# Performance work log

Hardware: AMD Instinct MI355X
Metric: run time of the kernel (lower is better)

The kernel has to match this reference:

```python
import jax, jax.numpy as jnp
import numpy as np

B, L, E, H = 2, 2048, 1024, 16
D = E // H  # head dim = 64


def setup_inputs() -> dict:
    key = jax.random.key(0)
    ks = jax.random.split(key, 10)
    s = 0.02
    return {
        "xt": jax.random.normal(ks[0], (B, L, E), jnp.float32),
        "xs": jax.random.normal(ks[1], (B, L, E), jnp.float32),
        "Wt": jax.random.normal(ks[2], (E, 3 * E), jnp.float32) * s,  # t_attn weight (x @ Wt)
        "bt": jnp.zeros((3 * E,), jnp.float32),
        "Ws": jax.random.normal(ks[3], (E, 2 * E), jnp.float32) * s,  # s_attn weight
        "bs": jnp.zeros((2 * E,), jnp.float32),
        "Wc": jax.random.normal(ks[4], (E, E), jnp.float32) * s,      # c_proj weight
        "bc": jnp.zeros((E,), jnp.float32),
        "lam_ts": jnp.ones((1,), jnp.float32),
        "lam_st": jnp.ones((1,), jnp.float32),
        "lam_ss": jnp.ones((1,), jnp.float32),
    }


def _heads(x):
    # (B, L, E) -> (B, H, L, D)
    return x.reshape(B, L, H, D).transpose(0, 2, 1, 3)


def reference(xt, xs, Wt, bt, Ws, bs, Wc, bc, lam_ts, lam_st, lam_ss):
    qt, kt, vt = jnp.split(xt @ Wt + bt, 3, axis=2)
    qs, ks = jnp.split(xs @ Ws + bs, 2, axis=2)
    qt, kt, vt, qs, ks = map(_heads, (qt, kt, vt, qs, ks))

    # 4-way disentangled scores; fuse the 4 matmuls into 2 by combining keys:
    # qt@kt^T + lam_ts*qt@ks^T = qt @ (kt + lam_ts*ks)^T
    # lam_st*qs@kt^T + lam_ss*qs@ks^T = qs @ (lam_st*kt + lam_ss*ks)^T
    k1 = kt + lam_ts[0] * ks
    k2 = lam_st[0] * kt + lam_ss[0] * ks
    att = (jnp.einsum('bhqd,bhkd->bhqk', qt, k1)
           + jnp.einsum('bhqd,bhkd->bhqk', qs, k2)) * (1.0 / np.sqrt(D))
    att = jax.nn.softmax(att, axis=-1)
    y = jnp.einsum('bhqk,bhkd->bhqd', att, vt)  # (B, H, L, D)
    y = y.transpose(0, 2, 1, 3).reshape(B, L, E)
    return y @ Wc + bc
```

## Files before the change

kernel.cpp:

```cpp
#include <hip/hip_runtime.h>
#include <math.h>

#define LQ 2048
#define EQ 1024
#define M_ROWS 4096
#define BH 32

typedef _Float16 f16x8 __attribute__((ext_vector_type(8)));
typedef _Float16 f16x4 __attribute__((ext_vector_type(4)));
typedef _Float16 f16x2 __attribute__((ext_vector_type(2)));
typedef float f32x4 __attribute__((ext_vector_type(4)));
typedef float f32x16 __attribute__((ext_vector_type(16)));

#define QSCALE 0.1803368801111204f

__device__ __forceinline__ void async_ld16(const _Float16* g, _Float16* l) {
  __builtin_amdgcn_global_load_lds(
      (const __attribute__((address_space(1))) unsigned int*)g,
      (__attribute__((address_space(3))) unsigned int*)l, 16, 0, 0);
}

__global__ __launch_bounds__(256) void prep(
    const float* __restrict__ xt, const float* __restrict__ xs,
    const float* __restrict__ Wt, const float* __restrict__ Ws,
    const float* __restrict__ Wc,
    _Float16* __restrict__ xt16, _Float16* __restrict__ xs16,
    _Float16* __restrict__ WtT, _Float16* __restrict__ WsT,
    _Float16* __restrict__ WcT) {
  int gb = blockIdx.x;
  if (gb < 4096) {
    int i = gb * 256 + threadIdx.x;
    const float* s; _Float16* d; size_t off;
    if (i < 524288) { s = xt; d = xt16; off = (size_t)i * 8; }
    else            { s = xs; d = xs16; off = (size_t)(i - 524288) * 8; }
    float4 a = *(const float4*)&s[off];
    float4 b = *(const float4*)&s[off + 4];
    f16x8 h;
    h[0] = (_Float16)a.x; h[1] = (_Float16)a.y; h[2] = (_Float16)a.z; h[3] = (_Float16)a.w;
    h[4] = (_Float16)b.x; h[5] = (_Float16)b.y; h[6] = (_Float16)b.z; h[7] = (_Float16)b.w;
    *(f16x8*)&d[off] = h;
  } else {
    __shared__ float T[32][65];
    int tb = gb - 4096;
    int c0 = (tb % 96) * 64;
    int k0 = (tb / 96) * 32;
    const float* W; _Float16* D; int Nw, cl;
    if (c0 < 3072)      { W = Wt; D = WtT; Nw = 3072; cl = c0; }
    else if (c0 < 5120) { W = Ws; D = WsT; Nw = 2048; cl = c0 - 3072; }
    else                { W = Wc; D = WcT; Nw = 1024; cl = c0 - 5120; }
    const int tid = threadIdx.x;
#pragma unroll
    for (int p = 0; p < 4; ++p) {
      int idx = tid + p * 256;
      int row = idx >> 5;
      int c2 = (idx & 31) * 2;
      float2 v = *(const float2*)&W[(size_t)(k0 + row) * Nw + cl + c2];
      T[row][c2] = v.x;
      T[row][c2 + 1] = v.y;
    }
    __syncthreads();
#pragma unroll
    for (int p = 0; p < 4; ++p) {
      int idx = tid + p * 256;
      int col = idx >> 4;
      int k2 = (idx & 15) * 2;
      f16x2 h2;
      h2[0] = (_Float16)T[k2][col];
      h2[1] = (_Float16)T[k2 + 1][col];
      *(f16x2*)&D[(size_t)(cl + col) * 1024 + k0 + k2] = h2;
    }
  }
}

__global__ __launch_bounds__(256, 3) void proj_gemm(
    const _Float16* __restrict__ xt16, const _Float16* __restrict__ xs16,
    const _Float16* __restrict__ WtT, const _Float16* __restrict__ WsT,
    const float* __restrict__ bt, const float* __restrict__ bs,
    _Float16* __restrict__ q16, _Float16* __restrict__ k16,
    _Float16* __restrict__ v16) {
  __shared__ _Float16 Al[128 * 64];
  __shared__ _Float16 Bl[128 * 64];

  const int tid = threadIdx.x;
  const int w = tid >> 6;
  const int lane = tid & 63;
  const int quad = lane >> 4;
  const int l15 = lane & 15;
  const int wm = w >> 1, wn = w & 1;
  const int by = blockIdx.y;
  const int n0 = blockIdx.x * 128;

  const _Float16* Ab;
  const _Float16* Bb;
  const float* bias;
  int m0, bsel = 0, branch;
  if (by < 32) {
    branch = 0; Ab = xt16; Bb = WtT; bias = bt; m0 = by * 128;
  } else if (by < 48) {
    branch = 1;
    int by2 = by - 32;
    bsel = by2 >> 3;
    m0 = (by2 & 7) * 128;
    Ab = WtT + (size_t)2048 * 1024;
    Bb = xt16 + (size_t)bsel * 2048 * 1024;
    bias = bt;
  } else {
    branch = 2; Ab = xs16; Bb = WsT; bias = bs; m0 = (by - 48) * 128;
  }

  const int srow = lane >> 3;
  const int sch = lane & 7;

  f32x4 acc[4][4];
#pragma unroll
  for (int mb = 0; mb < 4; ++mb)
#pragma unroll
    for (int nb = 0; nb < 4; ++nb) acc[mb][nb] = (f32x4){0.f, 0.f, 0.f, 0.f};

  for (int kt = 0; kt < 1024; kt += 64) {
    __syncthreads();
#pragma unroll
    for (int a = 0; a < 4; ++a) {
      int row = w * 32 + a * 8 + srow;
      int sc = sch ^ (row & 7);
      async_ld16(&Ab[(size_t)(m0 + row) * 1024 + kt + sc * 8], &Al[(w * 32 + a * 8) * 64]);
      async_ld16(&Bb[(size_t)(n0 + row) * 1024 + kt + sc * 8], &Bl[(w * 32 + a * 8) * 64]);
    }
    __syncthreads();

#pragma unroll
    for (int g = 0; g < 2; ++g) {
      f16x8 af[4], bf[4];
#pragma unroll
      for (int mb = 0; mb < 4; ++mb) {
        int row = wm * 64 + mb * 16 + l15;
        int pc = ((g * 4 + quad) ^ (row & 7)) * 8;
        af[mb] = *(const f16x8*)&Al[row * 64 + pc];
      }
#pragma unroll
      for (int nb = 0; nb < 4; ++nb) {
        int row = wn * 64 + nb * 16 + l15;
        int pc = ((g * 4 + quad) ^ (row & 7)) * 8;
        bf[nb] = *(const f16x8*)&Bl[row * 64 + pc];
      }
#pragma unroll
      for (int mb = 0; mb < 4; ++mb)
#pragma unroll
        for (int nb = 0; nb < 4; ++nb)
          acc[mb][nb] = __builtin_amdgcn_mfma_f32_16x16x32_f16(af[mb], bf[nb], acc[mb][nb], 0, 0, 0);
    }
  }

#pragma unroll
  for (int mb = 0; mb < 4; ++mb)
#pragma unroll
    for (int nb = 0; nb < 4; ++nb)
#pragma unroll
      for (int r = 0; r < 4; ++r) {
        int row = m0 + wm * 64 + mb * 16 + quad * 4 + r;
        int col = n0 + wn * 64 + nb * 16 + l15;
        if (branch == 1) {
          float val = acc[mb][nb][r] + bias[2048 + row];
          v16[(size_t)(bsel * 1024 + row) * 2048 + col] = (_Float16)val;
        } else {
          float val = acc[mb][nb][r] + bias[col];
          int bb = row >> 11, ll = row & 2047;
          int which = col >> 10, e = col & 1023;
          int hh = e >> 6, dd = e & 63;
          size_t rowhd = (size_t)(bb * 16 + hh) * 2048 + ll;
          int off = (branch == 0) ? 0 : 64;
          if (which == 0) q16[rowhd * 128 + off + dd] = (_Float16)val;
          else            k16[rowhd * 128 + off + dd] = (_Float16)val;
        }
      }
}

__global__ __launch_bounds__(256, 3) void cproj_gemm(
    const _Float16* __restrict__ A, const _Float16* __restrict__ Bm,
    const float* __restrict__ bias, float* __restrict__ outf) {
  __shared__ _Float16 Al0[128 * 32];
  __shared__ _Float16 Bl0[64 * 32];
  __shared__ _Float16 Al1[128 * 32];
  __shared__ _Float16 Bl1[64 * 32];

  const int tid = threadIdx.x;
  const int w = tid >> 6;
  const int lane = tid & 63;
  const int quad = lane >> 4;
  const int l15 = lane & 15;
  const int wm = w >> 1, wn = w & 1;
  const int m0 = blockIdx.y * 128;
  const int n0 = blockIdx.x * 64;

  const int srow = lane >> 2;
  const int schunk = ((lane & 3) ^ ((lane >> 3) & 3)) * 8;

  f32x4 acc[4][2];
#pragma unroll
  for (int mb = 0; mb < 4; ++mb)
#pragma unroll
    for (int nb = 0; nb < 2; ++nb) acc[mb][nb] = (f32x4){0.f, 0.f, 0.f, 0.f};

  const int key = (l15 >> 1) & 3;

  auto dma = [&](int kt, _Float16* Al, _Float16* Bl) {
#pragma unroll
    for (int i = 0; i < 2; ++i) {
      int rt = w * 32 + i * 16;
      async_ld16(&A[(size_t)(m0 + rt + srow) * 1024 + kt + schunk], &Al[rt * 32]);
    }
    int rtb = w * 16;
    async_ld16(&Bm[(size_t)(n0 + rtb + srow) * 1024 + kt + schunk], &Bl[rtb * 32]);
  };

  auto comp = [&](const _Float16* Al, const _Float16* Bl) {
    f16x8 af[4], bf[2];
    const int pc = (quad ^ key) * 8;
#pragma unroll
    for (int mb = 0; mb < 4; ++mb)
      af[mb] = *(const f16x8*)&Al[(wm * 64 + mb * 16 + l15) * 32 + pc];
#pragma unroll
    for (int nb = 0; nb < 2; ++nb)
      bf[nb] = *(const f16x8*)&Bl[(wn * 32 + nb * 16 + l15) * 32 + pc];
#pragma unroll
    for (int mb = 0; mb < 4; ++mb)
#pragma unroll
      for (int nb = 0; nb < 2; ++nb)
        acc[mb][nb] = __builtin_amdgcn_mfma_f32_16x16x32_f16(af[mb], bf[nb], acc[mb][nb], 0, 0, 0);
  };

  dma(0, Al0, Bl0);
  for (int kt = 0; kt < 1024; kt += 64) {
    __syncthreads();
    dma(kt + 32, Al1, Bl1);
    comp(Al0, Bl0);
    __syncthreads();
    if (kt + 64 < 1024) dma(kt + 64, Al0, Bl0);
    comp(Al1, Bl1);
  }

#pragma unroll
  for (int mb = 0; mb < 4; ++mb)
#pragma unroll
    for (int nb = 0; nb < 2; ++nb)
#pragma unroll
      for (int r = 0; r < 4; ++r) {
        int row = m0 + wm * 64 + mb * 16 + quad * 4 + r;
        int col = n0 + wn * 32 + nb * 16 + l15;
        outf[(size_t)row * 1024 + col] = acc[mb][nb][r] + bias[col];
      }
}

__global__ __launch_bounds__(256, 2) void flash_attn_mfma(
    const _Float16* __restrict__ qcat, const _Float16* __restrict__ kcat,
    const _Float16* __restrict__ vT, _Float16* __restrict__ y,
    const float* __restrict__ lam_ts, const float* __restrict__ lam_st,
    const float* __restrict__ lam_ss) {
  const int bh = blockIdx.y;
  const int qt0 = blockIdx.x * 128;
  const int b = bh >> 4, h = bh & 15;
  const _Float16* Qg = qcat + (size_t)bh * LQ * 128;
  const _Float16* Kg = kcat + (size_t)bh * LQ * 128;
  const _Float16* Vg = vT + (size_t)bh * 64 * LQ;

  __shared__ _Float16 Ksh0[64 * 128];
  __shared__ _Float16 Ksh1[64 * 128];
  __shared__ _Float16 Vsh0[64 * 64];
  __shared__ _Float16 Vsh1[64 * 64];

  const int tid = threadIdx.x;
  const int w = tid >> 6;
  const int lane = tid & 63;
  const int half = lane >> 5;
  const int l31 = lane & 31;

  const float lts = lam_ts[0], lst = lam_st[0], lss = lam_ss[0];

  f16x8 qf[8];
#pragma unroll
  for (int db = 0; db < 4; ++db) {
    const _Float16* qp = &Qg[(size_t)(qt0 + w * 32 + l31) * 128 + db * 16 + half * 8];
    f16x8 a = *(const f16x8*)qp;
    f16x8 bq = *(const f16x8*)(qp + 64);
#pragma unroll
    for (int e = 0; e < 8; ++e) {
      float fa = (float)a[e], fb = (float)bq[e];
      qf[db][e]     = (_Float16)(QSCALE * (fa + lst * fb));
      qf[db + 4][e] = (_Float16)(QSCALE * (lts * fa + lss * fb));
    }
  }

  float m_i = -INFINITY;
  float l_i = 0.f;
  f32x16 O[2];
#pragma unroll
  for (int nt = 0; nt < 2; ++nt)
#pragma unroll
    for (int r = 0; r < 16; ++r) O[nt][r] = 0.f;

  auto dma = [&](int t, _Float16* Kd, _Float16* Vd) {
#pragma unroll
    for (int a = 0; a < 4; ++a) {
      int row = w * 16 + a * 4 + (lane >> 4);
      int sc = (lane & 15) ^ (row & 7);
      async_ld16(&Kg[(size_t)(t + row) * 128 + sc * 8], &Kd[(w * 16 + a * 4) * 128]);
    }
#pragma unroll
    for (int a = 0; a < 2; ++a) {
      int row = w * 16 + a * 8 + (lane >> 3);
      int sc = (lane & 7) ^ (row & 7);
      async_ld16(&Vg[(size_t)row * LQ + t + sc * 8], &Vd[(w * 16 + a * 8) * 64]);
    }
  };

  auto compute = [&](const _Float16* Ks, const _Float16* Vs) {
    f32x16 S[2];
#pragma unroll
    for (int kb = 0; kb < 2; ++kb)
#pragma unroll
      for (int r = 0; r < 16; ++r) S[kb][r] = 0.f;
#pragma unroll
    for (int db = 0; db < 8; ++db) {
      const int pc = ((db * 2 + half) ^ (lane & 7)) * 8;
      f16x8 af[2];
#pragma unroll
      for (int kb = 0; kb < 2; ++kb)
        af[kb] = *(const f16x8*)&Ks[(kb * 32 + l31) * 128 + pc];
#pragma unroll
      for (int kb = 0; kb < 2; ++kb)
        S[kb] = __builtin_amdgcn_mfma_f32_32x32x16_f16(af[kb], qf[db], S[kb], 0, 0, 0);
    }

    float mx = -INFINITY;
#pragma unroll
    for (int kb = 0; kb < 2; ++kb)
#pragma unroll
      for (int r = 0; r < 16; ++r) mx = fmaxf(mx, S[kb][r]);
    mx = fmaxf(mx, __shfl_xor(mx, 32));
    float m_new = fmaxf(m_i, mx);
    float alpha = __builtin_amdgcn_exp2f(m_i - m_new);
    float s = 0.f;
#pragma unroll
    for (int kb = 0; kb < 2; ++kb)
#pragma unroll
      for (int r = 0; r < 16; ++r) {
        float p = __builtin_amdgcn_exp2f(S[kb][r] - m_new);
        S[kb][r] = p;
        s += p;
      }
    s += __shfl_xor(s, 32);
    l_i = l_i * alpha + s;
    m_i = m_new;

#pragma unroll
    for (int nt = 0; nt < 2; ++nt)
#pragma unroll
      for (int r = 0; r < 16; ++r) O[nt][r] *= alpha;

    unsigned pu[2][8];
#pragma unroll
    for (int kb = 0; kb < 2; ++kb)
#pragma unroll
      for (int i = 0; i < 8; ++i) {
        f16x2 t2;
        t2[0] = (_Float16)S[kb][2 * i];
        t2[1] = (_Float16)S[kb][2 * i + 1];
        pu[kb][i] = __builtin_bit_cast(unsigned, t2);
      }

#pragma unroll
    for (int kb = 0; kb < 2; ++kb)
#pragma unroll
      for (int c = 0; c < 2; ++c) {
        unsigned ulo0 = pu[kb][4 * c + 0], ulo1 = pu[kb][4 * c + 1];
        unsigned uhi0 = pu[kb][4 * c + 2], uhi1 = pu[kb][4 * c + 3];
        unsigned rlo0 = (unsigned)__shfl_xor((int)ulo0, 32);
        unsigned rlo1 = (unsigned)__shfl_xor((int)ulo1, 32);
        unsigned rhi0 = (unsigned)__shfl_xor((int)uhi0, 32);
        unsigned rhi1 = (unsigned)__shfl_xor((int)uhi1, 32);
        union { unsigned u[4]; f16x8 v; } pb;
        pb.u[0] = half ? rhi0 : ulo0;
        pb.u[1] = half ? rhi1 : ulo1;
        pb.u[2] = half ? uhi0 : rlo0;
        pb.u[3] = half ? uhi1 : rlo1;
        int kb2 = kb * 2 + c;
        f16x8 av[2];
#pragma unroll
        for (int nt = 0; nt < 2; ++nt) {
          int dim = nt * 32 + l31;
          int pc = ((kb2 * 2 + half) ^ (dim & 7)) * 8;
          av[nt] = *(const f16x8*)&Vs[dim * 64 + pc];
        }
#pragma unroll
        for (int nt = 0; nt < 2; ++nt)
          O[nt] = __builtin_amdgcn_mfma_f32_32x32x16_f16(av[nt], pb.v, O[nt], 0, 0, 0);
      }
  };

  dma(0, Ksh0, Vsh0);
  for (int t = 0; t < LQ; t += 128) {
    __syncthreads();
    dma(t + 64, Ksh1, Vsh1);
    compute(Ksh0, Vsh0);
    __syncthreads();
    if (t + 128 < LQ) dma(t + 128, Ksh0, Vsh0);
    compute(Ksh1, Vsh1);
  }

  float inv = 1.f / l_i;
  int qrow = qt0 + w * 32 + l31;
#pragma unroll
  for (int nt = 0; nt < 2; ++nt)
#pragma unroll
    for (int rg = 0; rg < 4; ++rg) {
      f16x4 o4;
#pragma unroll
      for (int i = 0; i < 4; ++i) o4[i] = (_Float16)(O[nt][rg * 4 + i] * inv);
      int dim = nt * 32 + rg * 8 + half * 4;
      *(f16x4*)&y[((size_t)b * LQ + qrow) * EQ + h * 64 + dim] = o4;
    }
}

extern "C" void kernel_launch(void* const* d_in, const int* in_sizes, int n_in,
                              void* d_out, int out_size, void* d_ws, size_t ws_size,
                              hipStream_t stream) {
  const float* xt = (const float*)d_in[0];
  const float* xs = (const float*)d_in[1];
  const float* Wt = (const float*)d_in[2];
  const float* bt = (const float*)d_in[3];
  const float* Ws = (const float*)d_in[4];
  const float* bs = (const float*)d_in[5];
  const float* Wc = (const float*)d_in[6];
  const float* bc = (const float*)d_in[7];
  const float* lam_ts = (const float*)d_in[8];
  const float* lam_st = (const float*)d_in[9];
  const float* lam_ss = (const float*)d_in[10];
  float* out = (float*)d_out;

  _Float16* w16 = (_Float16*)d_ws;
  _Float16* xt16 = w16;
  _Float16* xs16 = xt16 + 4194304;
  _Float16* WtT  = xs16 + 4194304;
  _Float16* WsT  = WtT + 3145728;
  _Float16* WcT  = WsT + 2097152;
  _Float16* qcat = WcT + 1048576;
  _Float16* kcat = qcat + 8388608;
  _Float16* vbufT = kcat + 8388608;
  _Float16* ybuf = vbufT + 4194304;

  prep<<<7168, 256, 0, stream>>>(xt, xs, Wt, Ws, Wc, xt16, xs16, WtT, WsT, WcT);
  proj_gemm<<<dim3(16, 80), 256, 0, stream>>>(
      xt16, xs16, WtT, WsT, bt, bs, qcat, kcat, vbufT);
  flash_attn_mfma<<<dim3(16, 32), 256, 0, stream>>>(
      qcat, kcat, vbufT, ybuf, lam_ts, lam_st, lam_ss);
  cproj_gemm<<<dim3(16, 32), 256, 0, stream>>>(ybuf, WcT, bc, out);
}
```

Baseline: 280.9 us.

## Process 128-key blocks per softmax step with deferred rescale and permlane swaps

The attention loop now does QK^T for two 64-key tiles before running one softmax/PV pass over 128 keys. This halves the number of max/rescale passes, and it adds two more V buffers so V tiles stay resident until the PV step. Rescaling of O and l is skipped unless some row max grows by more than a threshold (lazy rescale), and MFMA sections are raised in priority with s_setprio. The cross-half P shuffle now uses v_permlane32_swap instead of four shfl_xor plus selects. The cost is more registers (S[4]) and more LDS, which could lower occupancy.

```diff
diff --git a/kernel.cpp b/kernel.cpp
--- a/kernel.cpp
+++ b/kernel.cpp
@@ -13,6 +13,7 @@
 typedef float f32x16 __attribute__((ext_vector_type(16)));
 
 #define QSCALE 0.1803368801111204f
+#define DEFER_THR 8.0f
 
 __device__ __forceinline__ void async_ld16(const _Float16* g, _Float16* l) {
   __builtin_amdgcn_global_load_lds(
@@ -267,6 +268,8 @@
   __shared__ _Float16 Ksh1[64 * 128];
   __shared__ _Float16 Vsh0[64 * 64];
   __shared__ _Float16 Vsh1[64 * 64];
+  __shared__ _Float16 Vsh2[64 * 64];
+  __shared__ _Float16 Vsh3[64 * 64];
 
   const int tid = threadIdx.x;
   const int w = tid >> 6;
@@ -298,13 +301,15 @@
 #pragma unroll
     for (int r = 0; r < 16; ++r) O[nt][r] = 0.f;
 
-  auto dma = [&](int t, _Float16* Kd, _Float16* Vd) {
+  auto dma_k = [&](int t, _Float16* Kd) {
 #pragma unroll
     for (int a = 0; a < 4; ++a) {
       int row = w * 16 + a * 4 + (lane >> 4);
       int sc = (lane & 15) ^ (row & 7);
       async_ld16(&Kg[(size_t)(t + row) * 128 + sc * 8], &Kd[(w * 16 + a * 4) * 128]);
     }
+  };
+  auto dma_v = [&](int t, _Float16* Vd) {
 #pragma unroll
     for (int a = 0; a < 2; ++a) {
       int row = w * 16 + a * 8 + (lane >> 3);
@@ -313,98 +318,112 @@
     }
   };
 
-  auto compute = [&](const _Float16* Ks, const _Float16* Vs) {
-    f32x16 S[2];
-#pragma unroll
-    for (int kb = 0; kb < 2; ++kb)
-#pragma unroll
-      for (int r = 0; r < 16; ++r) S[kb][r] = 0.f;
+  auto qk = [&](const _Float16* Ks, f32x16* Sp) {
+    __builtin_amdgcn_s_setprio(1);
 #pragma unroll
     for (int db = 0; db < 8; ++db) {
       const int pc = ((db * 2 + half) ^ (lane & 7)) * 8;
-      f16x8 af[2];
-#pragma unroll
-      for (int kb = 0; kb < 2; ++kb)
-        af[kb] = *(const f16x8*)&Ks[(kb * 32 + l31) * 128 + pc];
-#pragma unroll
-      for (int kb = 0; kb < 2; ++kb)
-        S[kb] = __builtin_amdgcn_mfma_f32_32x32x16_f16(af[kb], qf[db], S[kb], 0, 0, 0);
-    }
-
+      f16x8 af0 = *(const f16x8*)&Ks[(l31) * 128 + pc];
+      f16x8 af1 = *(const f16x8*)&Ks[(32 + l31) * 128 + pc];
+      Sp[0] = __builtin_amdgcn_mfma_f32_32x32x16_f16(af0, qf[db], Sp[0], 0, 0, 0);
+      Sp[1] = __builtin_amdgcn_mfma_f32_32x32x16_f16(af1, qf[db], Sp[1], 0, 0, 0);
+    }
+    __builtin_amdgcn_s_setprio(0);
+  };
+
+  auto softpv = [&](f32x16* S, const _Float16* Vs0, const _Float16* Vs1) {
     float mx = -INFINITY;
 #pragma unroll
-    for (int kb = 0; kb < 2; ++kb)
+    for (int kb = 0; kb < 4; ++kb)
 #pragma unroll
       for (int r = 0; r < 16; ++r) mx = fmaxf(mx, S[kb][r]);
     mx = fmaxf(mx, __shfl_xor(mx, 32));
-    float m_new = fmaxf(m_i, mx);
-    float alpha = __builtin_amdgcn_exp2f(m_i - m_new);
+
+    if (__any(mx > m_i + DEFER_THR)) {
+      float m_new = fmaxf(m_i, mx);
+      float alpha = __builtin_amdgcn_exp2f(m_i - m_new);
+      l_i *= alpha;
+#pragma unroll
+      for (int nt = 0; nt < 2; ++nt)
+#pragma unroll
+        for (int r = 0; r < 16; ++r) O[nt][r] *= alpha;
+      m_i = m_new;
+    }
+
     float s = 0.f;
 #pragma unroll
-    for (int kb = 0; kb < 2; ++kb)
+    for (int kb = 0; kb < 4; ++kb)
 #pragma unroll
       for (int r = 0; r < 16; ++r) {
-        float p = __builtin_amdgcn_exp2f(S[kb][r] - m_new);
+        float p = __builtin_amdgcn_exp2f(S[kb][r] - m_i);
         S[kb][r] = p;
         s += p;
       }
     s += __shfl_xor(s, 32);
-    l_i = l_i * alpha + s;
-    m_i = m_new;
-
-#pragma unroll
-    for (int nt = 0; nt < 2; ++nt)
-#pragma unroll
-      for (int r = 0; r < 16; ++r) O[nt][r] *= alpha;
-
-    unsigned pu[2][8];
-#pragma unroll
-    for (int kb = 0; kb < 2; ++kb)
+    l_i += s;
+
+#pragma unroll
+    for (int kb = 0; kb < 4; ++kb) {
+      unsigned pu[8];
 #pragma unroll
       for (int i = 0; i < 8; ++i) {
         f16x2 t2;
         t2[0] = (_Float16)S[kb][2 * i];
         t2[1] = (_Float16)S[kb][2 * i + 1];
-        pu[kb][i] = __builtin_bit_cast(unsigned, t2);
-      }
-
-#pragma unroll
-    for (int kb = 0; kb < 2; ++kb)
+        pu[i] = __builtin_bit_cast(unsigned, t2);
+      }
 #pragma unroll
       for (int c = 0; c < 2; ++c) {
-        unsigned ulo0 = pu[kb][4 * c + 0], ulo1 = pu[kb][4 * c + 1];
-        unsigned uhi0 = pu[kb][4 * c + 2], uhi1 = pu[kb][4 * c + 3];
-        unsigned rlo0 = (unsigned)__shfl_xor((int)ulo0, 32);
-        unsigned rlo1 = (unsigned)__shfl_xor((int)ulo1, 32);
-        unsigned rhi0 = (unsigned)__shfl_xor((int)uhi0, 32);
-        unsigned rhi1 = (unsigned)__shfl_xor((int)uhi1, 32);
+        unsigned u0 = pu[4 * c + 0], u1 = pu[4 * c + 1];
+        unsigned u2 = pu[4 * c + 2], u3 = pu[4 * c + 3];
+        asm("v_permlane32_swap_b32 %0, %1" : "+v"(u0), "+v"(u2));
+        asm("v_permlane32_swap_b32 %0, %1" : "+v"(u1), "+v"(u3));
         union { unsigned u[4]; f16x8 v; } pb;
-        pb.u[0] = half ? rhi0 : ulo0;
-        pb.u[1] = half ? rhi1 : ulo1;
-        pb.u[2] = half ? uhi0 : rlo0;
-        pb.u[3] = half ? uhi1 : rlo1;
-        int kb2 = kb * 2 + c;
+        pb.u[0] = u0; pb.u[1] = u1; pb.u[2] = u2; pb.u[3] = u3;
+        const int kb2 = kb * 2 + c;
+        const _Float16* Vs = (kb2 < 4) ? Vs0 : Vs1;
+        const int kb2r = kb2 & 3;
         f16x8 av[2];
 #pragma unroll
         for (int nt = 0; nt < 2; ++nt) {
           int dim = nt * 32 + l31;
-          int pc = ((kb2 * 2 + half) ^ (dim & 7)) * 8;
+          int pc = ((kb2r * 2 + half) ^ (dim & 7)) * 8;
           av[nt] = *(const f16x8*)&Vs[dim * 64 + pc];
         }
+        __builtin_amdgcn_s_setprio(1);
 #pragma unroll
         for (int nt = 0; nt < 2; ++nt)
           O[nt] = __builtin_amdgcn_mfma_f32_32x32x16_f16(av[nt], pb.v, O[nt], 0, 0, 0);
-      }
-  };
-
-  dma(0, Ksh0, Vsh0);
-  for (int t = 0; t < LQ; t += 128) {
-    __syncthreads();
-    dma(t + 64, Ksh1, Vsh1);
-    compute(Ksh0, Vsh0);
-    __syncthreads();
-    if (t + 128 < LQ) dma(t + 128, Ksh0, Vsh0);
-    compute(Ksh1, Vsh1);
+        __builtin_amdgcn_s_setprio(0);
+      }
+    }
+  };
+
+  auto step = [&](int t, const _Float16* Vr0, _Float16* Vr1, _Float16* Vw2) {
+    f32x16 S[4];
+#pragma unroll
+    for (int kb = 0; kb < 4; ++kb)
+#pragma unroll
+      for (int r = 0; r < 16; ++r) S[kb][r] = 0.f;
+
+    __syncthreads();
+    dma_k(t + 64, Ksh1);
+    dma_v(t + 64, Vr1);
+    qk(Ksh0, &S[0]);
+    __syncthreads();
+    if (t + 128 < LQ) {
+      dma_k(t + 128, Ksh0);
+      dma_v(t + 128, Vw2);
+    }
+    qk(Ksh1, &S[2]);
+    softpv(S, Vr0, Vr1);
+  };
+
+  dma_k(0, Ksh0);
+  dma_v(0, Vsh0);
+  for (int t = 0; t < LQ; t += 256) {
+    step(t,       Vsh0, Vsh1, Vsh2);
+    step(t + 128, Vsh2, Vsh3, Vsh0);
   }
 
   float inv = 1.f / l_i;
```

Result: faster. 258.1 us (-8.1%).
